# Performance work log

Measured on AMD Instinct MI355X. Metric: run time of the kernel, lower is better.

## Reference

```python
import jax, jax.numpy as jnp
import numpy as np

B = 4096
NC = 64        # n_concepts
NT = 16        # n_tasks
H = 256        # prior_units (prior_layers = 1)
HID = 256      # prior_hids = [256, 256]
K = 20         # n_components
IN = 3 * NC + NT + 1        # GRU input size = 209
MLP_IN = H + 3 * NC + NT    # rnn_out input = 464
LOG_2PI = float(np.log(2.0 * np.pi))


def setup_inputs() -> dict:
    key = jax.random.key(0)
    ks = jax.random.split(key, 16)
    s = 0.05
    inp = {
        "z": jax.random.normal(ks[0], (B, NC), jnp.float32),
        "c": jax.random.normal(ks[1], (B, NC + NT), jnp.float32),
        "b": (jax.random.uniform(ks[2], (B, NC)) < 0.5).astype(jnp.float32),
        "m": (jax.random.uniform(ks[3], (B, NC)) < 0.5).astype(jnp.float32),
        # GRU (PyTorch layout: gates ordered r, z, n)
        "W_ih": jax.random.normal(ks[4], (3 * H, IN), jnp.float32) * s,
        "W_hh": jax.random.normal(ks[5], (3 * H, H), jnp.float32) * s,
        "b_ih": jax.random.normal(ks[6], (3 * H,), jnp.float32) * s,
        "b_hh": jax.random.normal(ks[7], (3 * H,), jnp.float32) * s,
        # rnn_out MLP: Linear(464,256)+Tanh, Linear(256,256)+Tanh, Linear(256,3K)
        "W1": jax.random.normal(ks[8], (HID, MLP_IN), jnp.float32) * s,
        "b1": jax.random.normal(ks[9], (HID,), jnp.float32) * s,
        "W2": jax.random.normal(ks[10], (HID, HID), jnp.float32) * s,
        "b2": jax.random.normal(ks[11], (HID,), jnp.float32) * s,
        "W3": jax.random.normal(ks[12], (3 * K, HID), jnp.float32) * s,
        "b3": jax.random.normal(ks[13], (3 * K,), jnp.float32) * s,
    }
    return inp


def _logp(z, c, b, m, W_ih, W_hh, b_ih, b_hh, W1, b1, W2, b2, W3, b3):
    Bsz, d = z.shape
    cbm = jnp.concatenate([c, b, m], axis=1)               # [B, 3*NC+NT]
    # z input at step t is -1 for t=0, else z[:, t-1]
    z_prev = jnp.concatenate(
        [-jnp.ones((Bsz, 1), z.dtype), z[:, :-1]], axis=1)  # [B, d]
    # Precompute the input-gate projections for all steps without
    # materializing the full [d, B, IN] sequence tensor:
    # column 0 of W_ih multiplies z_prev; the rest multiplies cbm.
    gi_cbm = cbm @ W_ih[:, 1:].T + b_ih                    # [B, 3H]
    gi = gi_cbm[None, :, :] + z_prev.T[:, :, None] * W_ih[:, 0][None, None, :]  # [d, B, 3H]

    def gru_step(h, gi_t):
        gh = h @ W_hh.T + b_hh
        gi_r, gi_u, gi_n = jnp.split(gi_t, 3, axis=-1)
        gh_r, gh_u, gh_n = jnp.split(gh, 3, axis=-1)
        r = jax.nn.sigmoid(gi_r + gh_r)
        u = jax.nn.sigmoid(gi_u + gh_u)
        n = jnp.tanh(gi_n + r * gh_n)
        h_new = (1.0 - u) * n + u * h
        return h_new, h_new

    h0 = jnp.zeros((Bsz, W_hh.shape[1]), z.dtype)
    _, hs = jax.lax.scan(gru_step, h0, gi)                 # [d, B, H]
    hs = jnp.transpose(hs, (1, 0, 2))                      # [B, d, H]

    feat = jnp.concatenate(
        [hs, jnp.broadcast_to(cbm[:, None, :], (Bsz, d, cbm.shape[1]))],
        axis=2)                                            # [B, d, MLP_IN]
    h1 = jnp.tanh(feat @ W1.T + b1)
    h2 = jnp.tanh(h1 @ W2.T + b2)
    params = h2 @ W3.T + b3                                # [B, d, 3K]

    logits, means, lsigmas = jnp.split(params, 3, axis=-1)
    t = z[..., None]                                       # [B, d, 1]
    log_norm = -lsigmas - 0.5 * LOG_2PI
    diff = (t - means) * jnp.exp(-lsigmas)
    log_kernel = -0.5 * jnp.square(diff)
    log_like = (jax.nn.logsumexp(log_kernel + log_norm + logits, axis=-1)
                - jax.nn.logsumexp(logits, axis=-1))       # [B, d]

    query = m * (1.0 - b)
    mask = jnp.sort(query, axis=1)[:, ::-1]                # descending sort of values
    return jnp.sum(log_like * mask, axis=1)                # [B]


def reference(z, c, b, m, W_ih, W_hh, b_ih, b_hh, W1, b1, W2, b2, W3, b3):
    return _logp(z, c, b, m, W_ih, W_hh, b_ih, b_hh,
                 W1, b1, W2, b2, W3, b3)
```

## Files before the change

kernel.cpp:

```cpp
#include <hip/hip_runtime.h>
#include <hip/hip_bf16.h>

#define BATCH  4096
#define NCC    64
#define HDIM   256
#define G3     768
#define NROW   (BATCH*NCC)
#define NK     20
#define LOG2PI 1.8378770664093453f

typedef __attribute__((ext_vector_type(8))) short bf16x8;
typedef __attribute__((ext_vector_type(4))) float f32x4;

__device__ __forceinline__ float sigm(float x) { return 1.0f/(1.0f + __expf(-x)); }
__device__ __forceinline__ float tanh_fast(float x) { return 1.0f - 2.0f/(__expf(2.0f*x) + 1.0f); }
__device__ __forceinline__ unsigned short f2bf(float x) {
  __hip_bfloat16 h = __float2bfloat16(x);
  return __builtin_bit_cast(unsigned short, h);
}
__device__ __forceinline__ int swz(int r) { return (r & 7) ^ ((r & 8) >> 2); }

__global__ __launch_bounds__(256) void k_cvtall(
    const float* __restrict__ c, const float* __restrict__ bv,
    const float* __restrict__ mv, const float* __restrict__ W_ih,
    const float* __restrict__ W_hh, const float* __restrict__ W1,
    const float* __restrict__ W2, const float* __restrict__ W3,
    unsigned short* __restrict__ cbmB, unsigned short* __restrict__ CW,
    unsigned short* __restrict__ WhhB, unsigned short* __restrict__ W1aB,
    unsigned short* __restrict__ W2B, unsigned short* __restrict__ W3pB,
    float* __restrict__ w0) {
  int idx = blockIdx.x*256 + threadIdx.x;
  if (idx < 1048576) {
    int row = idx >> 8, k = idx & 255;
    float v = 0.f;
    if (k < 80)       v = c [row*80 + k];
    else if (k < 144) v = bv[row*64 + (k-80)];
    else if (k < 208) v = mv[row*64 + (k-144)];
    cbmB[idx] = f2bf(v);
    return;
  }
  idx -= 1048576;
  if (idx < 262144) {
    int n = idx >> 8, k = idx & 255;
    float v = 0.f;
    if (n < 768) { if (k < 208) v = W_ih[n*209 + 1 + k]; }
    else         { if (k < 208) v = W1[(n-768)*464 + 256 + k]; }
    CW[idx] = f2bf(v);
    return;
  }
  idx -= 262144;
  if (idx < 196608) { WhhB[idx] = f2bf(W_hh[idx]); return; }
  idx -= 196608;
  if (idx < 65536) { int n = idx>>8, k = idx&255; W1aB[idx] = f2bf(W1[n*464+k]); return; }
  idx -= 65536;
  if (idx < 65536) { W2B[idx] = f2bf(W2[idx]); return; }
  idx -= 65536;
  if (idx < 16384) {
    int n = idx >> 8;
    float v = 0.f;
    if (n < 60) v = W3[idx];
    W3pB[idx] = f2bf(v);
    return;
  }
  idx -= 16384;
  if (idx < 768) w0[idx] = W_ih[idx*209];
}

__global__ __launch_bounds__(512) void k_pre(
    const unsigned short* __restrict__ A, const unsigned short* __restrict__ Bw,
    const float* __restrict__ b_ih, const float* __restrict__ b_hh,
    const float* __restrict__ b1,
    float* __restrict__ gi, float* __restrict__ P1) {
  __shared__ __align__(16) unsigned short As[128*64];
  __shared__ __align__(16) unsigned short Bs[128*64];
  int tid = threadIdx.x;
  int rb = blockIdx.x >> 3, cb = blockIdx.x & 7;
  long row0 = (long)rb * 128;
  int n0 = cb * 128;
  int wv = tid >> 6, lane = tid & 63;
  int lq = lane >> 4, l16 = lane & 15;
  int wrg = wv & 3, wcg = wv >> 2;
  f32x4 acc[2][4];
#pragma unroll
  for (int i = 0; i < 2; ++i)
#pragma unroll
    for (int j = 0; j < 4; ++j) acc[i][j] = (f32x4){0.f,0.f,0.f,0.f};
  for (int kb = 0; kb < 256; kb += 64) {
#pragma unroll
    for (int i = 0; i < 2; ++i) {
      int s = i*512 + tid;
      int r = s >> 3, cg = (s & 7) ^ (r & 7);
      *(uint4*)&As[s*8] = *(const uint4*)&A[(row0 + r)*256 + kb + cg*8];
      *(uint4*)&Bs[s*8] = *(const uint4*)&Bw[(long)(n0 + r)*256 + kb + cg*8];
    }
    __syncthreads();
#pragma unroll
    for (int kc = 0; kc < 2; ++kc) {
      int csel = kc*4 + lq;
      bf16x8 af[2];
#pragma unroll
      for (int rt = 0; rt < 2; ++rt) {
        int r = wrg*32 + rt*16 + l16;
        af[rt] = *(const bf16x8*)&As[r*64 + ((csel ^ (r & 7)))*8];
      }
#pragma unroll
      for (int ct = 0; ct < 4; ++ct) {
        int n = wcg*64 + ct*16 + l16;
        bf16x8 bfr = *(const bf16x8*)&Bs[n*64 + ((csel ^ (n & 7)))*8];
        acc[0][ct] = __builtin_amdgcn_mfma_f32_16x16x32_bf16(af[0], bfr, acc[0][ct], 0, 0, 0);
        acc[1][ct] = __builtin_amdgcn_mfma_f32_16x16x32_bf16(af[1], bfr, acc[1][ct], 0, 0, 0);
      }
    }
    __syncthreads();
  }
#pragma unroll
  for (int rt = 0; rt < 2; ++rt)
#pragma unroll
    for (int q = 0; q < 4; ++q) {
      long row = row0 + wrg*32 + rt*16 + lq*4 + q;
#pragma unroll
      for (int ct = 0; ct < 4; ++ct) {
        int n = n0 + wcg*64 + ct*16 + l16;
        float v = acc[rt][ct][q];
        if (n < 512)      gi[row*G3 + n] = v + b_ih[n] + b_hh[n];
        else if (n < 768) gi[row*G3 + n] = v + b_ih[n];
        else              P1[row*256 + (n-768)] = v + b1[n-768];
      }
    }
}

__global__ __attribute__((amdgpu_flat_work_group_size(1024, 1024)))
__attribute__((amdgpu_waves_per_eu(4, 4)))
void k_gru(
    const float* __restrict__ z, const float* __restrict__ gi,
    const unsigned short* __restrict__ WhhB, const float* __restrict__ b_hh,
    const float* __restrict__ w0, unsigned short* __restrict__ hs) {
  __shared__ __align__(16) unsigned short hbf[2*16*256];
  __shared__ __align__(16) float gis[768*20];
  __shared__ __align__(16) float zs[64*16];
  __shared__ float wls[768 + 256];
  int tid = threadIdx.x;
  int wv = tid >> 6, lane = tid & 63;
  int lq = lane >> 4, l16 = lane & 15;
  int row0 = blockIdx.x * 16;
  unsigned short* stg = (unsigned short*)gis;
  bf16x8 wf[3][8];
  for (int cg = 0; cg < 16; ++cg) {
    for (int s = tid; s < 1536; s += 1024) {
      int r = s >> 5, cc = s & 31;
      int g = r >> 4, col = r & 15;
      *(uint4*)&stg[r*256 + ((cc ^ (r & 7))*8)] =
          *(const uint4*)&WhhB[(long)(g*256 + cg*16 + col)*256 + cc*8];
    }
    __syncthreads();
    if (wv == cg) {
#pragma unroll
      for (int g = 0; g < 3; ++g)
#pragma unroll
        for (int ks = 0; ks < 8; ++ks) {
          int r = g*16 + l16, kc = ks*4 + lq;
          wf[g][ks] = *(const bf16x8*)&stg[r*256 + ((kc ^ (r & 7))*8)];
        }
    }
    __syncthreads();
  }
  if (tid < 768) wls[tid] = w0[tid];
  else if (tid < 1024) wls[tid] = b_hh[512 + (tid - 768)];
  {
    int t = tid >> 4, r = tid & 15;
    zs[tid] = z[(row0+r)*64 + t];
  }
#pragma unroll
  for (int i = 0; i < 12; ++i) {
    int s = i*1024 + tid;
    int r = s / 768, cc = s - r*768;
    gis[cc*20 + r] = gi[(long)(row0+r)*768 + cc];
  }
  for (int i = tid; i < 2048; i += 1024) ((unsigned int*)hbf)[i] = 0u;
  float hp[4] = {0.f, 0.f, 0.f, 0.f};
  const int s7 = l16 & 7;
  const int arow = l16*256;
  const int r4 = lq*4;
  const int hc = wv*16 + l16;
  const int cr = tid >> 6;
  const int c8 = (tid & 63) >> 1, half = tid & 1;
  const int csrc = cr*256 + ((c8 ^ (cr & 7))*8 + half*4);
  unsigned short* cbase = hs + (long)(row0+cr)*64*256 + c8*8 + half*4;
  __syncthreads();
#pragma unroll 1
  for (int t = 0; t < 64; ++t) {
    const int co = (t & 1) << 12;
    const int no = co ^ 4096;
    f32x4 a0, a1, a2;
    float zp[4];
    {
      float4 zv4 = *(const float4*)&zs[(t ? (t-1) : 0)*16 + r4];
      f32x4 gR = *(const f32x4*)&gis[hc*20 + r4];
      f32x4 gU = *(const f32x4*)&gis[(256+hc)*20 + r4];
      float w0r = wls[hc], w0u = wls[256+hc], bn = wls[768+hc];
#pragma unroll
      for (int q = 0; q < 4; ++q) {
        zp[q] = t ? (&zv4.x)[q] : -1.0f;
        a0[q] = gR[q] + zp[q]*w0r;
        a1[q] = gU[q] + zp[q]*w0u;
        a2[q] = bn;
      }
    }
#pragma unroll
    for (int ks = 0; ks < 8; ++ks) {
      bf16x8 af = *(const bf16x8*)&hbf[co + arow + (((ks*4+lq) ^ s7))*8];
      a0 = __builtin_amdgcn_mfma_f32_16x16x32_bf16(af, wf[0][ks], a0, 0, 0, 0);
      a1 = __builtin_amdgcn_mfma_f32_16x16x32_bf16(af, wf[1][ks], a1, 0, 0, 0);
      a2 = __builtin_amdgcn_mfma_f32_16x16x32_bf16(af, wf[2][ks], a2, 0, 0, 0);
    }
    if (t) {
      uint2 cd = *(const uint2*)&hbf[co + csrc];
      *(uint2*)(cbase + (t-1)*256) = cd;
    }
    {
      f32x4 gN = *(const f32x4*)&gis[(512+hc)*20 + r4];
      float w0n = wls[512+hc];
      int hchunk = hc >> 3, hlow = hc & 7;
#pragma unroll
      for (int q = 0; q < 4; ++q) {
        int r = r4 + q;
        float rr = sigm(a0[q]);
        float uu = sigm(a1[q]);
        float nn = tanh_fast(gN[q] + zp[q]*w0n + rr*a2[q]);
        float hn = uu*(hp[q] - nn) + nn;
        hp[q] = hn;
        hbf[no + r*256 + ((hchunk ^ (r & 7)))*8 + hlow] = f2bf(hn);
      }
    }
    __syncthreads();
  }
  uint2 cd = *(const uint2*)&hbf[0 + csrc];
  *(uint2*)(cbase + 63*256) = cd;
}

__global__ __launch_bounds__(512) void k_l1(
    const unsigned short* __restrict__ A, const unsigned short* __restrict__ Bw,
    const float* __restrict__ P1, unsigned short* __restrict__ Out) {
  __shared__ __align__(16) unsigned short As[128*64];
  __shared__ __align__(16) unsigned short Bs[256*64];
  int tid = threadIdx.x;
  long row0 = (long)blockIdx.x * 128;
  int wv = tid >> 6, lane = tid & 63;
  int lq = lane >> 4, l16 = lane & 15;
  int wrg = wv & 3, wcg = wv >> 2;
  f32x4 acc[2][8];
#pragma unroll
  for (int i = 0; i < 2; ++i)
#pragma unroll
    for (int j = 0; j < 8; ++j) acc[i][j] = (f32x4){0.f,0.f,0.f,0.f};
  for (int kb = 0; kb < 256; kb += 64) {
#pragma unroll
    for (int i = 0; i < 2; ++i) {
      int s = i*512 + tid;
      int r = s >> 3, cg = (s & 7) ^ (r & 7);
      *(uint4*)&As[s*8] = *(const uint4*)&A[(row0 + r)*256 + kb + cg*8];
    }
#pragma unroll
    for (int i = 0; i < 4; ++i) {
      int s = i*512 + tid;
      int r = s >> 3, cg = (s & 7) ^ (r & 7);
      *(uint4*)&Bs[s*8] = *(const uint4*)&Bw[(long)r*256 + kb + cg*8];
    }
    __syncthreads();
#pragma unroll
    for (int kc = 0; kc < 2; ++kc) {
      int csel = kc*4 + lq;
      bf16x8 af[2];
#pragma unroll
      for (int rt = 0; rt < 2; ++rt) {
        int r = wrg*32 + rt*16 + l16;
        af[rt] = *(const bf16x8*)&As[r*64 + ((csel ^ (r & 7)))*8];
      }
#pragma unroll
      for (int ct = 0; ct < 8; ++ct) {
        int n = wcg*128 + ct*16 + l16;
        bf16x8 bfr = *(const bf16x8*)&Bs[n*64 + ((csel ^ (n & 7)))*8];
        acc[0][ct] = __builtin_amdgcn_mfma_f32_16x16x32_bf16(af[0], bfr, acc[0][ct], 0, 0, 0);
        acc[1][ct] = __builtin_amdgcn_mfma_f32_16x16x32_bf16(af[1], bfr, acc[1][ct], 0, 0, 0);
      }
    }
    __syncthreads();
  }
#pragma unroll
  for (int rt = 0; rt < 2; ++rt)
#pragma unroll
    for (int q = 0; q < 4; ++q) {
      long row = row0 + wrg*32 + rt*16 + lq*4 + q;
#pragma unroll
      for (int ct = 0; ct < 8; ++ct) {
        int n = wcg*128 + ct*16 + l16;
        float b = P1[(row >> 6)*256 + n];
        Out[row*256 + n] = f2bf(tanh_fast(acc[rt][ct][q] + b));
      }
    }
}

__global__ __launch_bounds__(512) void k_l23(
    const unsigned short* __restrict__ A, const unsigned short* __restrict__ W2B,
    const float* __restrict__ b2, const unsigned short* __restrict__ W3pB,
    const float* __restrict__ b3, const float* __restrict__ z,
    float* __restrict__ ll) {
  __shared__ __align__(16) unsigned short As[128*64];
  __shared__ __align__(16) unsigned short Bs[256*64];
  __shared__ __align__(16) unsigned short h2s[128*256];
  int tid = threadIdx.x;
  long row0 = (long)blockIdx.x * 128;
  int wv = tid >> 6, lane = tid & 63;
  int lq = lane >> 4, l16 = lane & 15;
  int wrg = wv & 3, wcg = wv >> 2;
  f32x4 acc[2][8];
#pragma unroll
  for (int i = 0; i < 2; ++i)
#pragma unroll
    for (int j = 0; j < 8; ++j) acc[i][j] = (f32x4){0.f,0.f,0.f,0.f};
  for (int kb = 0; kb < 256; kb += 64) {
#pragma unroll
    for (int i = 0; i < 2; ++i) {
      int s = i*512 + tid;
      int r = s >> 3, cg = (s & 7) ^ (r & 7);
      *(uint4*)&As[s*8] = *(const uint4*)&A[(row0 + r)*256 + kb + cg*8];
    }
#pragma unroll
    for (int i = 0; i < 4; ++i) {
      int s = i*512 + tid;
      int r = s >> 3, cg = (s & 7) ^ (r & 7);
      *(uint4*)&Bs[s*8] = *(const uint4*)&W2B[(long)r*256 + kb + cg*8];
    }
    __syncthreads();
#pragma unroll
    for (int kc = 0; kc < 2; ++kc) {
      int csel = kc*4 + lq;
      bf16x8 af[2];
#pragma unroll
      for (int rt = 0; rt < 2; ++rt) {
        int r = wrg*32 + rt*16 + l16;
        af[rt] = *(const bf16x8*)&As[r*64 + ((csel ^ (r & 7)))*8];
      }
#pragma unroll
      for (int ct = 0; ct < 8; ++ct) {
        int n = wcg*128 + ct*16 + l16;
        bf16x8 bfr = *(const bf16x8*)&Bs[n*64 + ((csel ^ (n & 7)))*8];
        acc[0][ct] = __builtin_amdgcn_mfma_f32_16x16x32_bf16(af[0], bfr, acc[0][ct], 0, 0, 0);
        acc[1][ct] = __builtin_amdgcn_mfma_f32_16x16x32_bf16(af[1], bfr, acc[1][ct], 0, 0, 0);
      }
    }
    __syncthreads();
  }
#pragma unroll
  for (int rt = 0; rt < 2; ++rt)
#pragma unroll
    for (int q = 0; q < 4; ++q) {
      int lr = wrg*32 + rt*16 + lq*4 + q;
#pragma unroll
      for (int ct = 0; ct < 8; ++ct) {
        int n = wcg*128 + ct*16 + l16;
        h2s[lr*256 + (((n >> 3) ^ swz(lr))*8 + (n & 7))] =
            f2bf(tanh_fast(acc[rt][ct][q] + b2[n]));
      }
    }
#pragma unroll
  for (int i = 0; i < 4; ++i) {
    int s = i*512 + tid;
    int r = s >> 5, cc = s & 31;
    *(uint4*)&Bs[r*256 + ((cc ^ swz(r)))*8] = *(const uint4*)&W3pB[r*256 + cc*8];
  }
  __syncthreads();
  f32x4 pacc[4];
#pragma unroll
  for (int j = 0; j < 4; ++j) pacc[j] = (f32x4){0.f,0.f,0.f,0.f};
#pragma unroll
  for (int ks = 0; ks < 8; ++ks) {
    int chunk = ks*4 + lq;
    int ar = wv*16 + l16;
    bf16x8 af = *(const bf16x8*)&h2s[ar*256 + ((chunk ^ swz(ar)))*8];
#pragma unroll
    for (int ct = 0; ct < 4; ++ct) {
      int br = ct*16 + l16;
      bf16x8 bfr = *(const bf16x8*)&Bs[br*256 + ((chunk ^ swz(br)))*8];
      pacc[ct] = __builtin_amdgcn_mfma_f32_16x16x32_bf16(af, bfr, pacc[ct], 0, 0, 0);
    }
  }
  float* Ps = (float*)&h2s[wv*16*256];
#pragma unroll
  for (int ct = 0; ct < 4; ++ct) {
    int n = ct*16 + l16;
    float b = (n < 60) ? b3[n] : 0.0f;
#pragma unroll
    for (int q = 0; q < 4; ++q)
      Ps[(lq*4 + q)*68 + n] = pacc[ct][q] + b;
  }
  if (lane < 16) {
    long grow = row0 + wv*16 + lane;
    float zv = z[grow];
    const float* p = &Ps[lane*68];
    float mx1 = -1e30f;
#pragma unroll
    for (int i = 0; i < NK; ++i) mx1 = fmaxf(mx1, p[i]);
    float s1 = 0.0f;
#pragma unroll
    for (int i = 0; i < NK; ++i) s1 += __expf(p[i] - mx1);
    float lse1 = mx1 + __logf(s1);
    float a[NK];
    float mx2 = -1e30f;
#pragma unroll
    for (int i = 0; i < NK; ++i) {
      float lg = p[i], me = p[20+i], ls = p[40+i];
      float e = __expf(-ls);
      float d = (zv - me) * e;
      float ai = -0.5f*d*d - ls - 0.5f*LOG2PI + lg;
      a[i] = ai;
      mx2 = fmaxf(mx2, ai);
    }
    float s2 = 0.0f;
#pragma unroll
    for (int i = 0; i < NK; ++i) s2 += __expf(a[i] - mx2);
    float lse2 = mx2 + __logf(s2);
    ll[grow] = lse2 - lse1;
  }
}

__global__ __launch_bounds__(256) void k_final(const float* __restrict__ bv,
    const float* __restrict__ mv, const float* __restrict__ ll,
    float* __restrict__ out) {
  int tid = threadIdx.x;
  int wave = tid >> 6, lane = tid & 63;
  int b = blockIdx.x*4 + wave;
  float q = mv[b*64 + lane] * (1.0f - bv[b*64 + lane]);
  unsigned long long bal = __ballot(q > 0.5f);
  int S = __popcll(bal);
  float val = (lane < S) ? ll[(long)b*64 + lane] : 0.0f;
#pragma unroll
  for (int off = 32; off > 0; off >>= 1) val += __shfl_down(val, off);
  if (lane == 0) out[b] = val;
}

extern "C" void kernel_launch(void* const* d_in, const int* in_sizes, int n_in,
                              void* d_out, int out_size, void* d_ws, size_t ws_size,
                              hipStream_t stream) {
  const float* z    = (const float*)d_in[0];
  const float* c    = (const float*)d_in[1];
  const float* bv   = (const float*)d_in[2];
  const float* mv   = (const float*)d_in[3];
  const float* W_ih = (const float*)d_in[4];
  const float* W_hh = (const float*)d_in[5];
  const float* b_ih = (const float*)d_in[6];
  const float* b_hh = (const float*)d_in[7];
  const float* W1   = (const float*)d_in[8];
  const float* b1   = (const float*)d_in[9];
  const float* W2   = (const float*)d_in[10];
  const float* b2   = (const float*)d_in[11];
  const float* W3   = (const float*)d_in[12];
  const float* b3   = (const float*)d_in[13];
  float* out = (float*)d_out;

  char* p = (char*)d_ws;
  auto alloc = [&](size_t bytes) {
    char* q = p;
    p += (bytes + 255) & ~(size_t)255;
    return q;
  };
  unsigned short* cbmB = (unsigned short*)alloc((size_t)BATCH*256*2);
  unsigned short* CW   = (unsigned short*)alloc((size_t)1024*256*2);
  unsigned short* WhhB = (unsigned short*)alloc((size_t)G3*256*2);
  unsigned short* W1aB = (unsigned short*)alloc((size_t)256*256*2);
  unsigned short* W2B  = (unsigned short*)alloc((size_t)256*256*2);
  unsigned short* W3pB = (unsigned short*)alloc((size_t)64*256*2);
  float* w0 = (float*)alloc((size_t)G3*4);
  float* gi = (float*)alloc((size_t)BATCH*G3*4);
  float* P1 = (float*)alloc((size_t)BATCH*256*4);
  float* ll = (float*)alloc((size_t)NROW*4);
  unsigned short* hs = (unsigned short*)alloc((size_t)NROW*HDIM*2);

  k_cvtall<<<6468, 256, 0, stream>>>(c, bv, mv, W_ih, W_hh, W1, W2, W3,
                                     cbmB, CW, WhhB, W1aB, W2B, W3pB, w0);
  k_pre<<<256, 512, 0, stream>>>(cbmB, CW, b_ih, b_hh, b1, gi, P1);
  k_gru<<<256, 1024, 0, stream>>>(z, gi, WhhB, b_hh, w0, hs);
  k_l1<<<NROW/128, 512, 0, stream>>>(hs, W1aB, P1, hs);
  k_l23<<<NROW/128, 512, 0, stream>>>(hs, W2B, b2, W3pB, b3, z, ll);
  k_final<<<BATCH/4, 256, 0, stream>>>(bv, mv, ll, out);
}
```

Measured before the change: 562.2 us.

## Process 32 rows per GRU block, stream W_hh from global, store gi as bf16

New measurement: 957.9 us. +70.4%, slower.

```diff
diff --git a/kernel.cpp b/kernel.cpp
--- a/kernel.cpp
+++ b/kernel.cpp
@@ -17,6 +17,10 @@
 __device__ __forceinline__ unsigned short f2bf(float x) {
   __hip_bfloat16 h = __float2bfloat16(x);
   return __builtin_bit_cast(unsigned short, h);
+}
+__device__ __forceinline__ float bf2f(unsigned short u) {
+  unsigned int v = ((unsigned int)u) << 16;
+  return __builtin_bit_cast(float, v);
 }
 __device__ __forceinline__ int swz(int r) { return (r & 7) ^ ((r & 8) >> 2); }
 
@@ -130,112 +134,105 @@
 }
 
 __global__ __attribute__((amdgpu_flat_work_group_size(1024, 1024)))
-__attribute__((amdgpu_waves_per_eu(4, 4)))
 void k_gru(
     const float* __restrict__ z, const float* __restrict__ gi,
     const unsigned short* __restrict__ WhhB, const float* __restrict__ b_hh,
     const float* __restrict__ w0, unsigned short* __restrict__ hs) {
-  __shared__ __align__(16) unsigned short hbf[2*16*256];
-  __shared__ __align__(16) float gis[768*20];
-  __shared__ __align__(16) float zs[64*16];
-  __shared__ float wls[768 + 256];
+  __shared__ __align__(16) unsigned short hbf[2*32*256];
+  __shared__ __align__(16) unsigned short gis[768*36];
+  __shared__ __align__(16) float zs[64*32];
+  __shared__ float wls[1024];
   int tid = threadIdx.x;
   int wv = tid >> 6, lane = tid & 63;
   int lq = lane >> 4, l16 = lane & 15;
-  int row0 = blockIdx.x * 16;
-  unsigned short* stg = (unsigned short*)gis;
-  bf16x8 wf[3][8];
-  for (int cg = 0; cg < 16; ++cg) {
-    for (int s = tid; s < 1536; s += 1024) {
-      int r = s >> 5, cc = s & 31;
-      int g = r >> 4, col = r & 15;
-      *(uint4*)&stg[r*256 + ((cc ^ (r & 7))*8)] =
-          *(const uint4*)&WhhB[(long)(g*256 + cg*16 + col)*256 + cc*8];
-    }
-    __syncthreads();
-    if (wv == cg) {
-#pragma unroll
-      for (int g = 0; g < 3; ++g)
-#pragma unroll
-        for (int ks = 0; ks < 8; ++ks) {
-          int r = g*16 + l16, kc = ks*4 + lq;
-          wf[g][ks] = *(const bf16x8*)&stg[r*256 + ((kc ^ (r & 7))*8)];
-        }
-    }
-    __syncthreads();
-  }
+  int row0 = blockIdx.x * 32;
+  const int hc = wv*16 + l16;
+  const unsigned short* bp0 = WhhB + (long)(         hc)*256 + lq*8;
+  const unsigned short* bp1 = WhhB + (long)(256 +    hc)*256 + lq*8;
+  const unsigned short* bp2 = WhhB + (long)(512 +    hc)*256 + lq*8;
   if (tid < 768) wls[tid] = w0[tid];
-  else if (tid < 1024) wls[tid] = b_hh[512 + (tid - 768)];
-  {
-    int t = tid >> 4, r = tid & 15;
-    zs[tid] = z[(row0+r)*64 + t];
-  }
-#pragma unroll
-  for (int i = 0; i < 12; ++i) {
+  else           wls[tid] = b_hh[512 + (tid - 768)];
+  for (int i = tid; i < 2048; i += 1024) {
+    int t = i >> 5, r = i & 31;
+    zs[i] = z[(row0 + r)*64 + t];
+  }
+#pragma unroll
+  for (int i = 0; i < 24; ++i) {
     int s = i*1024 + tid;
     int r = s / 768, cc = s - r*768;
-    gis[cc*20 + r] = gi[(long)(row0+r)*768 + cc];
-  }
-  for (int i = tid; i < 2048; i += 1024) ((unsigned int*)hbf)[i] = 0u;
-  float hp[4] = {0.f, 0.f, 0.f, 0.f};
+    gis[cc*36 + r] = f2bf(gi[(long)(row0 + r)*768 + cc]);
+  }
+  for (int i = tid; i < 4096; i += 1024) ((unsigned int*)hbf)[i] = 0u;
+  float hp[2][4] = {{0.f,0.f,0.f,0.f},{0.f,0.f,0.f,0.f}};
   const int s7 = l16 & 7;
-  const int arow = l16*256;
   const int r4 = lq*4;
-  const int hc = wv*16 + l16;
-  const int cr = tid >> 6;
-  const int c8 = (tid & 63) >> 1, half = tid & 1;
-  const int csrc = cr*256 + ((c8 ^ (cr & 7))*8 + half*4);
-  unsigned short* cbase = hs + (long)(row0+cr)*64*256 + c8*8 + half*4;
+  const int cr = tid >> 5, ccc = tid & 31;
+  const int csrc = cr*256 + ((ccc ^ (cr & 7)))*8;
+  unsigned short* cbase = hs + (long)(row0 + cr)*64*256 + ccc*8;
   __syncthreads();
 #pragma unroll 1
   for (int t = 0; t < 64; ++t) {
-    const int co = (t & 1) << 12;
-    const int no = co ^ 4096;
-    f32x4 a0, a1, a2;
-    float zp[4];
+    const int co = (t & 1) << 13;
+    const int no = co ^ 8192;
+    f32x4 a[6];
+    float zp[2][4];
     {
-      float4 zv4 = *(const float4*)&zs[(t ? (t-1) : 0)*16 + r4];
-      f32x4 gR = *(const f32x4*)&gis[hc*20 + r4];
-      f32x4 gU = *(const f32x4*)&gis[(256+hc)*20 + r4];
       float w0r = wls[hc], w0u = wls[256+hc], bn = wls[768+hc];
-#pragma unroll
-      for (int q = 0; q < 4; ++q) {
-        zp[q] = t ? (&zv4.x)[q] : -1.0f;
-        a0[q] = gR[q] + zp[q]*w0r;
-        a1[q] = gU[q] + zp[q]*w0u;
-        a2[q] = bn;
+      int tm = (t ? (t-1) : 0)*32;
+#pragma unroll
+      for (int rt = 0; rt < 2; ++rt) {
+        float4 zv4 = *(const float4*)&zs[tm + rt*16 + r4];
+        const unsigned short* gb = &gis[hc*36 + rt*16 + r4];
+#pragma unroll
+        for (int q = 0; q < 4; ++q) {
+          float zpv = t ? (&zv4.x)[q] : -1.0f;
+          zp[rt][q] = zpv;
+          a[rt][q]   = bf2f(gb[q + 0*(256*36 - 0)]) + zpv*w0r;
+          a[2+rt][q] = bf2f(gis[(256+hc)*36 + rt*16 + r4 + q]) + zpv*w0u;
+          a[4+rt][q] = bn;
+        }
       }
     }
 #pragma unroll
     for (int ks = 0; ks < 8; ++ks) {
-      bf16x8 af = *(const bf16x8*)&hbf[co + arow + (((ks*4+lq) ^ s7))*8];
-      a0 = __builtin_amdgcn_mfma_f32_16x16x32_bf16(af, wf[0][ks], a0, 0, 0, 0);
-      a1 = __builtin_amdgcn_mfma_f32_16x16x32_bf16(af, wf[1][ks], a1, 0, 0, 0);
-      a2 = __builtin_amdgcn_mfma_f32_16x16x32_bf16(af, wf[2][ks], a2, 0, 0, 0);
+      bf16x8 b0 = *(const bf16x8*)(bp0 + ks*32);
+      bf16x8 b1 = *(const bf16x8*)(bp1 + ks*32);
+      bf16x8 b2 = *(const bf16x8*)(bp2 + ks*32);
+#pragma unroll
+      for (int rt = 0; rt < 2; ++rt) {
+        int r = rt*16 + l16;
+        bf16x8 af = *(const bf16x8*)&hbf[co + r*256 + (((ks*4+lq) ^ (r & 7)))*8];
+        a[rt]   = __builtin_amdgcn_mfma_f32_16x16x32_bf16(af, b0, a[rt],   0, 0, 0);
+        a[2+rt] = __builtin_amdgcn_mfma_f32_16x16x32_bf16(af, b1, a[2+rt], 0, 0, 0);
+        a[4+rt] = __builtin_amdgcn_mfma_f32_16x16x32_bf16(af, b2, a[4+rt], 0, 0, 0);
+      }
     }
     if (t) {
-      uint2 cd = *(const uint2*)&hbf[co + csrc];
-      *(uint2*)(cbase + (t-1)*256) = cd;
+      uint4 cd = *(const uint4*)&hbf[co + csrc];
+      *(uint4*)(cbase + (t-1)*256) = cd;
     }
     {
-      f32x4 gN = *(const f32x4*)&gis[(512+hc)*20 + r4];
       float w0n = wls[512+hc];
       int hchunk = hc >> 3, hlow = hc & 7;
 #pragma unroll
-      for (int q = 0; q < 4; ++q) {
-        int r = r4 + q;
-        float rr = sigm(a0[q]);
-        float uu = sigm(a1[q]);
-        float nn = tanh_fast(gN[q] + zp[q]*w0n + rr*a2[q]);
-        float hn = uu*(hp[q] - nn) + nn;
-        hp[q] = hn;
-        hbf[no + r*256 + ((hchunk ^ (r & 7)))*8 + hlow] = f2bf(hn);
-      }
-    }
-    __syncthreads();
-  }
-  uint2 cd = *(const uint2*)&hbf[0 + csrc];
-  *(uint2*)(cbase + 63*256) = cd;
+      for (int rt = 0; rt < 2; ++rt) {
+#pragma unroll
+        for (int q = 0; q < 4; ++q) {
+          int lr = rt*16 + r4 + q;
+          float rr = sigm(a[rt][q]);
+          float uu = sigm(a[2+rt][q]);
+          float gn = bf2f(gis[(512+hc)*36 + lr]);
+          float nn = tanh_fast(gn + zp[rt][q]*w0n + rr*a[4+rt][q]);
+          float hn = uu*(hp[rt][q] - nn) + nn;
+          hp[rt][q] = hn;
+          hbf[no + lr*256 + ((hchunk ^ (lr & 7)))*8 + hlow] = f2bf(hn);
+        }
+      }
+    }
+    __syncthreads();
+  }
+  uint4 cd = *(const uint4*)&hbf[0 + csrc];
+  *(uint4*)(cbase + 63*256) = cd;
 }
 
 __global__ __launch_bounds__(512) void k_l1(
@@ -479,7 +476,7 @@
   k_cvtall<<<6468, 256, 0, stream>>>(c, bv, mv, W_ih, W_hh, W1, W2, W3,
                                      cbmB, CW, WhhB, W1aB, W2B, W3pB, w0);
   k_pre<<<256, 512, 0, stream>>>(cbmB, CW, b_ih, b_hh, b1, gi, P1);
-  k_gru<<<256, 1024, 0, stream>>>(z, gi, WhhB, b_hh, w0, hs);
+  k_gru<<<128, 1024, 0, stream>>>(z, gi, WhhB, b_hh, w0, hs);
   k_l1<<<NROW/128, 512, 0, stream>>>(hs, W1aB, P1, hs);
   k_l23<<<NROW/128, 512, 0, stream>>>(hs, W2B, b2, W3pB, b3, z, ll);
   k_final<<<BATCH/4, 256, 0, stream>>>(bv, mv, ll, out);
```
